# Kernel optimization log

Hardware: AMD Instinct MI355X
Metric: run time of the kernel (lower is better)

Reference implementation:

```python
import jax, jax.numpy as jnp
import numpy as np

N = 50000   # nodes (= node_input)
H = 128     # node_hidden
E = 800000  # edges per adjacency


def spmm(row, col, val, dense):
    # (sparse NxN) @ dense[N, F] via gather + segment_sum
    return jax.ops.segment_sum(dense[col] * val[:, None], row, num_segments=N)


def l2norm(x, eps=1e-12):
    n = jnp.sqrt(jnp.sum(x * x, axis=1, keepdims=True))
    return x / jnp.maximum(n, eps)


def setup_inputs() -> dict:
    key = jax.random.key(0)
    ks = jax.random.split(key, 20)
    stdv = 1.0 / np.sqrt(H)
    u = lambda k, shape, s: jax.random.uniform(k, shape, jnp.float32, -s, s)
    inp = {
        'in_row': jax.random.randint(ks[0], (E,), 0, N),
        'in_col': jax.random.randint(ks[1], (E,), 0, N),
        'in_val': jax.random.uniform(ks[2], (E,), jnp.float32),
        'out_row': jax.random.randint(ks[3], (E,), 0, N),
        'out_col': jax.random.randint(ks[4], (E,), 0, N),
        'out_val': jax.random.uniform(ks[5], (E,), jnp.float32),
        'W1': u(ks[6], (N, H), stdv), 'b1': u(ks[7], (H,), stdv),
        'W2': u(ks[8], (H, H), stdv), 'b2': u(ks[9], (H,), stdv),
        'W3': u(ks[10], (H, H), stdv), 'b3': u(ks[11], (H,), stdv),
        'W4': u(ks[12], (H, H), stdv), 'b4': u(ks[13], (H,), stdv),
        'lin1_w': jax.random.normal(ks[14], (2 * H, H), jnp.float32) * 0.05,
        'lin1_b': jnp.zeros((2 * H,), jnp.float32),
        'lin2_w': jax.random.normal(ks[15], (2 * H, 2 * H), jnp.float32) * 0.05,
        'lin2_b': jnp.zeros((2 * H,), jnp.float32),
        'lin3_w': jax.random.normal(ks[16], (1, 2 * H), jnp.float32) * 0.05,
        'lin3_b': jnp.zeros((1,), jnp.float32),
    }
    return inp


def reference(in_row, in_col, in_val, out_row, out_col, out_val,
              W1, b1, W2, b2, W3, b3, W4, b4,
              lin1_w, lin1_b, lin2_w, lin2_b, lin3_w, lin3_b):
    def branch(row, col, val):
        x1 = l2norm(jax.nn.relu(spmm(row, col, val, W1) + b1))
        x2 = l2norm(jax.nn.relu(spmm(row, col, val, x1 @ W2) + b2))
        x3 = l2norm(jax.nn.relu(spmm(row, col, val, x2 @ W3) + b3))
        x4 = jax.nn.relu(spmm(row, col, val, x3 @ W4) + b4)
        return (x1, x2, x3, x4)

    def score(x):  # dropout p=0.0 -> identity
        h = jax.nn.relu(x @ lin1_w.T + lin1_b)
        h = jax.nn.relu(h @ lin2_w.T + lin2_b)
        return h @ lin3_w.T + lin3_b

    xs_in = branch(in_row, in_col, in_val)
    xs_out = branch(out_row, out_col, out_val)
    score_in = sum(score(x) for x in xs_in)
    score_out = sum(score(x) for x in xs_out)
    return score_in * score_out
```

## Files before the change

### kernel.cpp

```cpp
#include <hip/hip_runtime.h>
#include <hip/hip_bf16.h>

#define NN 50000
#define HH 128
#define H2 256
#define EE 800000
#define NBUCK 196
#define BINCH 4096

typedef _Float16 half8 __attribute__((ext_vector_type(8)));
typedef float float4v __attribute__((ext_vector_type(4)));

__device__ __forceinline__ float bf2f(unsigned short u) {
  union { unsigned int i; float f; } v; v.i = ((unsigned int)u) << 16; return v.f;
}
__device__ __forceinline__ unsigned short f2bf(float f) {
  union { float f; unsigned int i; } v; v.f = f;
  unsigned int x = v.i;
  unsigned int r = x + 0x7fffu + ((x >> 16) & 1u);
  return (unsigned short)(r >> 16);
}

__global__ void detect_kernel(const unsigned int* __restrict__ val, int* __restrict__ dt) {
  unsigned int w = val[threadIdx.x];
  unsigned short u = (unsigned short)(w & 0xffff);
  int expf = (u >> 7) & 0xff;
  bool match = ((u >> 15) == 0) && expf >= 0x5A && expf <= 0x7E;
  unsigned long long m = __ballot(match);
  if (threadIdx.x == 0) dt[0] = (__popcll(m) >= 48) ? 1 : 0;
}

#define NSEG 14
struct ConvSegs {
  const void* s[NSEG];
  void* d[NSEG];
  int n[NSEG];
  int mode[NSEG];
  int kd[NSEG];
  int bstart[NSEG + 1];
};

__global__ __launch_bounds__(256) void convall_kernel(ConvSegs cs, const int* __restrict__ dt) {
  int b = blockIdx.x;
  int seg = 0;
  while (b >= cs.bstart[seg + 1]) ++seg;
  int i = (b - cs.bstart[seg]) * 256 + threadIdx.x;
  if (i >= cs.n[seg]) return;
  float f = dt[0] ? bf2f(((const unsigned short*)cs.s[seg])[i])
                  : ((const float*)cs.s[seg])[i];
  int m = cs.mode[seg];
  if (m == 0) { ((float*)cs.d[seg])[i] = f; return; }
  if (m == 1) { ((_Float16*)cs.d[seg])[i] = (_Float16)f; return; }
  int K = cs.kd[seg];
  int n, k;
  if (m == 3) { n = i / K; k = i - n * K; }
  else        { k = i >> 7; n = i & 127; }
  int NC16 = (cs.n[seg] / K) >> 4;
  int off = ((k >> 5) * NC16 + (n >> 4)) * 512 + (((k >> 3) & 3) * 16 + (n & 15)) * 8 + (k & 7);
  ((_Float16*)cs.d[seg])[off] = (_Float16)f;
}

__global__ __launch_bounds__(256) void bincount_kernel(
    const int* __restrict__ r0, const int* __restrict__ r1,
    int* __restrict__ bcnt, int E) {
  int br = blockIdx.y;
  const int* rows = br ? r1 : r0;
  __shared__ int cnt_s[NBUCK];
  int t = threadIdx.x;
  for (int i = t; i < NBUCK; i += 256) cnt_s[i] = 0;
  __syncthreads();
  int e0 = blockIdx.x * BINCH;
  #pragma unroll
  for (int i = 0; i < 16; ++i) {
    int e = e0 + i * 256 + t;
    if (e < E) atomicAdd(&cnt_s[rows[e] >> 8], 1);
  }
  __syncthreads();
  for (int i = t; i < NBUCK; i += 256) {
    int c = cnt_s[i];
    if (c) atomicAdd(&bcnt[br * NBUCK + i], c);
  }
}

// ... 70 lines not shown
  int* r = rp + br * (NN + 1);
  __shared__ int cur[256];
  __shared__ int s[256];
  int base = bbase[br * NBUCK + b];
  int end  = (b + 1 < NBUCK) ? bbase[br * NBUCK + b + 1] : E;
  cur[t] = 0;
  __syncthreads();
  for (int i = base + t; i < end; i += 256)
    atomicAdd(&cur[(((unsigned)bin[i].x) >> 16) & 255], 1);
  __syncthreads();
  int v = cur[t];
  s[t] = v;
  __syncthreads();
  for (int off = 1; off < 256; off <<= 1) {
    int u = (t >= off) ? s[t - off] : 0;
    __syncthreads();
    s[t] += u;
    __syncthreads();
  }
  int ex = base + s[t] - v;
  int row = b * 256 + t;
  if (row < N) r[row] = ex;
  if (b == 0 && t == 0) r[N] = E;
  cur[t] = ex;
  __syncthreads();
  for (int i = base + t; i < end; i += 256) {
    int2 e = bin[i];
    int rl = (((unsigned)e.x) >> 16) & 255;
    int p = atomicAdd(&cur[rl], 1);
    eo[p] = make_int2(e.x & 0xffff, e.y);
  }
}

template<int DO_L2>
__global__ __launch_bounds__(256) void spmm_kernel(
    const int* __restrict__ rp, const int2* __restrict__ edges,
    const _Float16* __restrict__ src, size_t sstride, const float* __restrict__ bias,
    _Float16* __restrict__ dst, size_t dstride, int N)
{
  int br = blockIdx.y;
  rp += br * (NN + 1);
  edges += (size_t)br * EE;
  src += br * sstride;
  dst += br * dstride;
  int g = threadIdx.x >> 4;
  int l = threadIdx.x & 15;
  int r = blockIdx.x * 16 + g;
  if (r >= N) return;
  int kb = rp[r], ke = rp[r + 1];
  float a0[8] = {0,0,0,0,0,0,0,0}, a1[8] = {0,0,0,0,0,0,0,0};
  float a2[8] = {0,0,0,0,0,0,0,0}, a3[8] = {0,0,0,0,0,0,0,0};
  int k = kb;
  for (; k + 3 < ke; k += 4) {
    int2 e0 = edges[k], e1 = edges[k + 1], e2 = edges[k + 2], e3 = edges[k + 3];
    half8 s0 = *(const half8*)(src + (size_t)e0.x * HH + l * 8);
    half8 s1 = *(const half8*)(src + (size_t)e1.x * HH + l * 8);
    half8 s2 = *(const half8*)(src + (size_t)e2.x * HH + l * 8);
    half8 s3 = *(const half8*)(src + (size_t)e3.x * HH + l * 8);
    float v0 = __int_as_float(e0.y), v1 = __int_as_float(e1.y);
    float v2 = __int_as_float(e2.y), v3 = __int_as_float(e3.y);
    #pragma unroll
    for (int j = 0; j < 8; ++j) {
      a0[j] = fmaf(v0, (float)s0[j], a0[j]);
      a1[j] = fmaf(v1, (float)s1[j], a1[j]);
      a2[j] = fmaf(v2, (float)s2[j], a2[j]);
      a3[j] = fmaf(v3, (float)s3[j], a3[j]);
    }
  }
  for (; k < ke; ++k) {
    int2 e0 = edges[k];
    half8 s0 = *(const half8*)(src + (size_t)e0.x * HH + l * 8);
    float v0 = __int_as_float(e0.y);
    #pragma unroll
    for (int j = 0; j < 8; ++j) a0[j] = fmaf(v0, (float)s0[j], a0[j]);
  }
  float x[8];
  #pragma unroll
  for (int j = 0; j < 8; ++j)
    x[j] = fmaxf((a0[j] + a1[j]) + (a2[j] + a3[j]) + bias[l * 8 + j], 0.f);
  if (DO_L2) {
    float ss = 0.f;
    #pragma unroll
    for (int j = 0; j < 8; ++j) ss += x[j] * x[j];
    #pragma unroll
    for (int m = 1; m < 16; m <<= 1) ss += __shfl_xor(ss, m, 64);
    float sc = 1.f / fmaxf(sqrtf(ss), 1e-12f);
    #pragma unroll
    for (int j = 0; j < 8; ++j) x[j] *= sc;
  }
  half8 hv;
  #pragma unroll
  for (int j = 0; j < 8; ++j) hv[j] = (_Float16)x[j];
  *(half8*)&dst[(size_t)r * HH + l * 8] = hv;
}

template<int DO_L2>
__global__ __launch_bounds__(256, 6) void fused_kernel(
    const int* __restrict__ rp, const int2* __restrict__ edges,
    const _Float16* __restrict__ xcur, _Float16* __restrict__ xnext,
    const _Float16* __restrict__ wt, const float* __restrict__ bias,
    const _Float16* __restrict__ w1, const _Float16* __restrict__ w2,
    const float* __restrict__ b1v, const float* __restrict__ b2v,
    const float* __restrict__ w3v,
    float* __restrict__ S, int N, int sg, int gx, int nsp)
{
  extern __shared__ _Float16 smem[];
  const size_t XSC = (size_t)(NN + 128) * HH;
  int br = blockIdx.y;
  rp += br * (NN + 1);
  edges += (size_t)br * EE;
  xcur += br * XSC;

  int bx = blockIdx.x;
  int role, idx;
  if (nsp) {
    int q = bx / 3, k3 = bx - q * 3;
    if (k3 < 2) { idx = q * 2 + k3; if (idx >= sg) return; role = 0; }
    else        { idx = q;          if (idx >= gx) return; role = 1; }
  } else { role = 1; idx = bx; if (idx >= gx) return; }

  const int lane = threadIdx.x & 63, w = threadIdx.x >> 6;
  const int lm = lane & 15, lq = lane >> 4;

  if (role == 0) {
    xnext += br * XSC;
    int g = threadIdx.x >> 4, l = threadIdx.x & 15;
    int r = idx * 16 + g;
    int kb = rp[r], ke = rp[r + 1];
    float a0[8] = {0,0,0,0,0,0,0,0}, a1[8] = {0,0,0,0,0,0,0,0};
    float a2[8] = {0,0,0,0,0,0,0,0}, a3[8] = {0,0,0,0,0,0,0,0};
    int k = kb;
    for (; k + 3 < ke; k += 4) {
      int2 e0 = edges[k], e1 = edges[k + 1], e2 = edges[k + 2], e3 = edges[k + 3];
      half8 s0 = *(const half8*)(xcur + (size_t)e0.x * HH + l * 8);
      half8 s1 = *(const half8*)(xcur + (size_t)e1.x * HH + l * 8);
      half8 s2 = *(const half8*)(xcur + (size_t)e2.x * HH + l * 8);
      half8 s3 = *(const half8*)(xcur + (size_t)e3.x * HH + l * 8);
      float v0 = __int_as_float(e0.y), v1 = __int_as_float(e1.y);
      float v2 = __int_as_float(e2.y), v3 = __int_as_float(e3.y);
      #pragma unroll
      for (int j = 0; j < 8; ++j) {
        a0[j] = fmaf(v0, (float)s0[j], a0[j]);
        a1[j] = fmaf(v1, (float)s1[j], a1[j]);
        a2[j] = fmaf(v2, (float)s2[j], a2[j]);
        a3[j] = fmaf(v3, (float)s3[j], a3[j]);
      }
    }
    for (; k < ke; ++k) {
      int2 e0 = edges[k];
      half8 s0 = *(const half8*)(xcur + (size_t)e0.x * HH + l * 8);
      float v0 = __int_as_float(e0.y);
      #pragma unroll
      for (int j = 0; j < 8; ++j) a0[j] = fmaf(v0, (float)s0[j], a0[j]);
    }
    half8 hv;
    #pragma unroll
    for (int j = 0; j < 8; ++j)
      hv[j] = (_Float16)((a0[j] + a1[j]) + (a2[j] + a3[j]));
    *(half8*)&smem[g * 136 + l * 8] = hv;
    __syncthreads();

    float4v acc[2];
    acc[0] = (float4v){0.f,0.f,0.f,0.f};
    acc[1] = (float4v){0.f,0.f,0.f,0.f};
    #pragma unroll
    for (int k0 = 0; k0 < HH; k0 += 32) {
      half8 ah = *(const half8*)&smem[lm * 136 + k0 + lq * 8];
      #pragma unroll
      for (int nt = 0; nt < 2; ++nt) {
        half8 bh = *(const half8*)(wt + (((k0 >> 5) * 8) + w * 2 + nt) * 512 + lane * 8);
        acc[nt] = __builtin_amdgcn_mfma_f32_16x16x32_f16(ah, bh, acc[nt], 0, 0, 0);
      }
    }
    float v[2][4];
    float ssp[4] = {0.f, 0.f, 0.f, 0.f};
    #pragma unroll
    for (int nt = 0; nt < 2; ++nt) {
      float bv = bias[w * 32 + nt * 16 + lm];
      #pragma unroll
      for (int rr = 0; rr < 4; ++rr) {
        float t = fmaxf(acc[nt][rr] + bv, 0.f);
        v[nt][rr] = t;
        ssp[rr] += t * t;
      }
    }
    if (DO_L2) {
      #pragma unroll
      for (int m = 1; m < 16; m <<= 1) {
        #pragma unroll
        for (int rr = 0; rr < 4; ++rr) ssp[rr] += __shfl_xor(ssp[rr], m, 64);
      }
      float* sred = (float*)(smem + 16 * 136);
      if (lm == 0) {
        #pragma unroll
        for (int rr = 0; rr < 4; ++rr) sred[w * 16 + lq * 4 + rr] = ssp[rr];
      }
      __syncthreads();
      #pragma unroll
      for (int rr = 0; rr < 4; ++rr) {
        int rowl = lq * 4 + rr;
        float tot = sred[rowl] + sred[16 + rowl] + sred[32 + rowl] + sred[48 + rowl];
        float sc = 1.f / fmaxf(sqrtf(tot), 1e-12f);
        v[0][rr] *= sc;
        v[1][rr] *= sc;
      }
    }
    #pragma unroll
    for (int rr = 0; rr < 4; ++rr) {
      size_t ro = (size_t)(idx * 16 + lq * 4 + rr) * HH;
      #pragma unroll
      for (int nt = 0; nt < 2; ++nt)
        xnext[ro + w * 32 + nt * 16 + lm] = (_Float16)v[nt][rr];
    }
    return;
  }

  float* Sb = S + (size_t)br * N;
  _Float16* h1s = smem;
  const int HS = H2 + 8;
  const int m0 = idx * 32;
  const int wn = w * 64;
  {
    float4v acc[2][4];
    #pragma unroll
    for (int i = 0; i < 2; ++i)
      #pragma unroll
      for (int j = 0; j < 4; ++j) acc[i][j] = (float4v){0.f,0.f,0.f,0.f};
    #pragma unroll
    for (int k0 = 0; k0 < HH; k0 += 32) {
      half8 ah[2], bh[4];
      #pragma unroll
      for (int mt = 0; mt < 2; ++mt)
        ah[mt] = *(const half8*)(xcur + (size_t)(m0 + mt * 16 + lm) * HH + k0 + lq * 8);
      #pragma unroll
      for (int nt = 0; nt < 4; ++nt)
        bh[nt] = *(const half8*)(w1 + (((k0 >> 5) * 16) + (wn >> 4) + nt) * 512 + lane * 8);
      #pragma unroll
      for (int mt = 0; mt < 2; ++mt)
        #pragma unroll
        for (int nt = 0; nt < 4; ++nt)
          acc[mt][nt] = __builtin_amdgcn_mfma_f32_16x16x32_f16(ah[mt], bh[nt], acc[mt][nt], 0, 0, 0);
    }
    float bv[4];
    #pragma unroll
    for (int nt = 0; nt < 4; ++nt) bv[nt] = b1v[wn + nt * 16 + lm];
// ... 60 lines not shown
                             const int* __restrict__ dt) {
  int i = blockIdx.x * 256 + threadIdx.x;
  if (i >= N) return;
  float b = 4.f * b3[0];
  float v = (s_in[i] + b) * (s_out[i] + b);
  if (dt[0]) ((unsigned short*)out)[i] = f2bf(v);
  else       ((float*)out)[i] = v;
}

extern "C" void kernel_launch(void* const* d_in, const int* in_sizes, int n_in,
                              void* d_out, int out_size, void* d_ws, size_t ws_size,
                              hipStream_t stream) {
  const int N = NN, E = EE;

  char* ws = (char*)d_ws;
  size_t o = 0;
  auto alloc = [&](size_t bytes) -> void* {
    void* p = ws + o;
    o = (o + bytes + 255) & ~(size_t)255;
    return p;
  };

  int* dt = (int*)alloc(16);
  float* bc[4]; float* l1b; float* l2b; float* w3f; float* l3b;
  for (int i = 0; i < 4; ++i) bc[i] = (float*)alloc(HH * 4);
  l1b = (float*)alloc(H2 * 4);
  l2b = (float*)alloc(H2 * 4);
  w3f = (float*)alloc(H2 * 4);
  l3b = (float*)alloc(4);
  _Float16* l1w_h = (_Float16*)alloc(H2 * HH * 2);
  _Float16* l2w_h = (_Float16*)alloc(H2 * H2 * 2);
  _Float16* Wt_h[3];
  for (int i = 0; i < 3; ++i) Wt_h[i] = (_Float16*)alloc(HH * HH * 2);
  _Float16* w1_h = (_Float16*)alloc((size_t)N * HH * 2);

  const int NP = N + 128;
  const size_t XS = (size_t)NP * HH;
  int* rp    = (int*)alloc(2 * (size_t)(N + 1) * 4);
  int* bcnt  = (int*)alloc(2 * NBUCK * 4);
  int* bbase = (int*)alloc(2 * NBUCK * 4);
  int* gcur  = (int*)alloc(2 * NBUCK * 4);
  int2* binned = (int2*)alloc(2 * (size_t)E * 8);
  int2* edges  = (int2*)alloc(2 * (size_t)E * 8);
  _Float16* x_h  = (_Float16*)alloc(2 * XS * 2);
  _Float16* tb_h = (_Float16*)alloc(2 * XS * 2);
  float* sacc = (float*)alloc(2 * (size_t)N * 4);

  dim3 blk(256);
  detect_kernel<<<1, 64, 0, stream>>>((const unsigned int*)d_in[2], dt);

  ConvSegs cs;
  const void* srcs[NSEG] = {d_in[7], d_in[9], d_in[11], d_in[13], d_in[15], d_in[17],
                            d_in[18], d_in[19], d_in[14], d_in[16], d_in[8], d_in[10],
                            d_in[12], d_in[6]};
  void* dsts[NSEG] = {bc[0], bc[1], bc[2], bc[3], l1b, l2b, w3f, l3b,
                      l1w_h, l2w_h, Wt_h[0], Wt_h[1], Wt_h[2], w1_h};
  int ns[NSEG] = {HH, HH, HH, HH, H2, H2, H2, 1,
                  H2 * HH, H2 * H2, HH * HH, HH * HH, HH * HH, N * HH};
  int ms[NSEG] = {0, 0, 0, 0, 0, 0, 0, 0, 3, 3, 4, 4, 4, 1};
  int ks[NSEG] = {0, 0, 0, 0, 0, 0, 0, 0, HH, H2, HH, HH, HH, 0};
  int btot = 0;
  for (int i = 0; i < NSEG; ++i) {
    cs.s[i] = srcs[i]; cs.d[i] = dsts[i]; cs.n[i] = ns[i]; cs.mode[i] = ms[i]; cs.kd[i] = ks[i];
    cs.bstart[i] = btot;
    btot += (ns[i] + 255) / 256;
  }
  cs.bstart[NSEG] = btot;
  convall_kernel<<<btot, blk, 0, stream>>>(cs, dt);

  hipMemsetAsync(sacc, 0, 2 * (size_t)N * 4, stream);
  hipMemsetAsync(bcnt, 0, 2 * NBUCK * 4, stream);
  hipMemsetAsync(x_h  + (size_t)N * HH, 0, (size_t)128 * HH * 2, stream);
  hipMemsetAsync(x_h  + XS + (size_t)N * HH, 0, (size_t)128 * HH * 2, stream);
  hipMemsetAsync(tb_h + (size_t)N * HH, 0, (size_t)128 * HH * 2, stream);
  hipMemsetAsync(tb_h + XS + (size_t)N * HH, 0, (size_t)128 * HH * 2, stream);

  int sg   = (N + 15) / 16;
  int gx32 = (N + 31) / 32;
  int mg   = ((sg + 1) / 2) * 3;
  int bg   = (E + BINCH - 1) / BINCH;
  const size_t FLDS = (size_t)32 * (H2 + 8) * sizeof(_Float16);

  bincount_kernel<<<dim3(bg, 2), blk, 0, stream>>>((const int*)d_in[0], (const int*)d_in[3], bcnt, E);
  bscan_kernel<<<dim3(1, 2), blk, 0, stream>>>(bcnt, bbase, gcur);
  bin_kernel<<<dim3(bg, 2), blk, 0, stream>>>(
      (const int*)d_in[0], (const int*)d_in[3], (const int*)d_in[1], (const int*)d_in[4],
      d_in[2], d_in[5], gcur, binned, E, dt);
  bucket_kernel<<<dim3(NBUCK, 2), blk, 0, stream>>>(bbase, binned, edges, rp, N, E);

  spmm_kernel<1><<<dim3(sg, 2), blk, 0, stream>>>(rp, edges, w1_h, 0, bc[0], x_h, XS, N);

  fused_kernel<1><<<dim3(mg, 2), blk, FLDS, stream>>>(
      rp, edges, x_h, tb_h, Wt_h[0], bc[1], l1w_h, l2w_h, l1b, l2b, w3f,
      sacc, N, sg, gx32, 1);
  fused_kernel<1><<<dim3(mg, 2), blk, FLDS, stream>>>(
      rp, edges, tb_h, x_h, Wt_h[1], bc[2], l1w_h, l2w_h, l1b, l2b, w3f,
      sacc, N, sg, gx32, 1);
  fused_kernel<0><<<dim3(mg, 2), blk, FLDS, stream>>>(
      rp, edges, x_h, tb_h, Wt_h[2], bc[3], l1w_h, l2w_h, l1b, l2b, w3f,
      sacc, N, sg, gx32, 1);
  fused_kernel<0><<<dim3(gx32, 2), blk, FLDS, stream>>>(
      rp, edges, tb_h, nullptr, nullptr, nullptr, l1w_h, l2w_h, l1b, l2b, w3f,
      sacc, N, 0, gx32, 0);

  final_kernel<<<(N + 255) / 256, blk, 0, stream>>>(sacc, sacc + N, l3b, d_out, N, dt);
}
```

Before: 560.1 us.

## Gather SpMM sources from packed 12-bit fp16 copies with fp16 packed math

Adds a 12-bit-per-element packed copy of each feature matrix (an 8-bit high byte plus a 4-bit nibble, 192 bytes per row instead of 256), written next to the fp16 output. The SpMM gathers now read this compressed form and accumulate with packed half2 multiplies. This cuts gather bandwidth, the dominant cost of the random-access SpMM. The gather-and-transform role is also retiled to 32 rows per block with 8 lanes per row, using 2x2 MFMA tiles. In exchange the inputs lose mantissa precision and sums are partly formed in fp16, which risks accuracy tolerance, and each layer now writes an extra quantized copy.

```diff
diff --git a/kernel.cpp b/kernel.cpp
--- a/kernel.cpp
+++ b/kernel.cpp
@@ -7,8 +7,10 @@
 #define EE 800000
 #define NBUCK 196
 #define BINCH 4096
+#define QS 192
 
 typedef _Float16 half8 __attribute__((ext_vector_type(8)));
+typedef _Float16 half2v __attribute__((ext_vector_type(2)));
 typedef float float4v __attribute__((ext_vector_type(4)));
 
 __device__ __forceinline__ float bf2f(unsigned short u) {
@@ -19,6 +21,109 @@
   unsigned int x = v.i;
   unsigned int r = x + 0x7fffu + ((x >> 16) & 1u);
   return (unsigned short)(r >> 16);
+}
+
+__device__ __forceinline__ unsigned int enc12h(unsigned short h) {
+  unsigned int m = (unsigned int)h & 0x7fffu;
+  unsigned int c = (m + 0x7u + ((h >> 4) & 1u)) >> 4;
+  return c | (((unsigned int)h >> 15) << 11);
+}
+__device__ __forceinline__ unsigned int enc12f(float x) {
+  return enc12h(__builtin_bit_cast(unsigned short, (_Float16)x));
+}
+
+__device__ __forceinline__ void dec8(unsigned int hw0, unsigned int hw1, unsigned int nw,
+                                     half2v vv, half2v& p0, half2v& p1,
+                                     half2v& p2, half2v& p3) {
+  unsigned int u01 = __byte_perm(hw0, 0u, 0x4140);
+  unsigned int u23 = __byte_perm(hw0, 0u, 0x4342);
+  unsigned int u45 = __byte_perm(hw1, 0u, 0x4140);
+  unsigned int u67 = __byte_perm(hw1, 0u, 0x4342);
+  unsigned int a01 = ((nw & 0xFu) << 4)        | ((nw & 0xF0u) << 16);
+  unsigned int a23 = ((nw & 0xF00u) >> 4)      | ((nw & 0xF000u) << 8);
+  unsigned int a45 = ((nw & 0xF0000u) >> 12)   | (nw & 0xF00000u);
+  unsigned int a67 = ((nw & 0x0F000000u) >> 20) | ((nw & 0xF0000000u) >> 8);
+  p0 += __builtin_bit_cast(half2v, (u01 << 8) | a01) * vv;
+  p1 += __builtin_bit_cast(half2v, (u23 << 8) | a23) * vv;
+  p2 += __builtin_bit_cast(half2v, (u45 << 8) | a45) * vv;
+  p3 += __builtin_bit_cast(half2v, (u67 << 8) | a67) * vv;
+}
+
+__device__ __forceinline__ void gather_q12(int kb, int ke,
+    const int2* __restrict__ edges, const unsigned char* __restrict__ sq,
+    int l, float* a)
+{
+  int k = kb;
+  for (; k + 3 < ke; k += 4) {
+    int2 e0 = edges[k], e1 = edges[k + 1], e2 = edges[k + 2], e3 = edges[k + 3];
+    const unsigned char* b0 = sq + (size_t)e0.x * QS;
+    const unsigned char* b1 = sq + (size_t)e1.x * QS;
+    const unsigned char* b2 = sq + (size_t)e2.x * QS;
+    const unsigned char* b3 = sq + (size_t)e3.x * QS;
+    uint4 Ha = *(const uint4*)(b0 + l * 16);
+    uint4 Hb = *(const uint4*)(b1 + l * 16);
+    uint4 Hc = *(const uint4*)(b2 + l * 16);
+    uint4 Hd = *(const uint4*)(b3 + l * 16);
+    uint2 La = *(const uint2*)(b0 + 128 + l * 8);
+    uint2 Lb = *(const uint2*)(b1 + 128 + l * 8);
+    uint2 Lc = *(const uint2*)(b2 + 128 + l * 8);
+    uint2 Ld = *(const uint2*)(b3 + 128 + l * 8);
+    _Float16 v0 = (_Float16)__int_as_float(e0.y);
+    _Float16 v1 = (_Float16)__int_as_float(e1.y);
+    _Float16 v2 = (_Float16)__int_as_float(e2.y);
+    _Float16 v3 = (_Float16)__int_as_float(e3.y);
+    half2v vv0 = {v0, v0}, vv1 = {v1, v1}, vv2 = {v2, v2}, vv3 = {v3, v3};
+    half2v p0 = {0, 0}, p1 = {0, 0}, p2 = {0, 0}, p3 = {0, 0};
+    half2v p4 = {0, 0}, p5 = {0, 0}, p6 = {0, 0}, p7 = {0, 0};
+    dec8(Ha.x, Ha.y, La.x, vv0, p0, p1, p2, p3);
+    dec8(Ha.z, Ha.w, La.y, vv0, p4, p5, p6, p7);
+    dec8(Hb.x, Hb.y, Lb.x, vv1, p0, p1, p2, p3);
+    dec8(Hb.z, Hb.w, Lb.y, vv1, p4, p5, p6, p7);
+    dec8(Hc.x, Hc.y, Lc.x, vv2, p0, p1, p2, p3);
+    dec8(Hc.z, Hc.w, Lc.y, vv2, p4, p5, p6, p7);
+    dec8(Hd.x, Hd.y, Ld.x, vv3, p0, p1, p2, p3);
+    dec8(Hd.z, Hd.w, Ld.y, vv3, p4, p5, p6, p7);
+    a[0] += (float)p0[0]; a[1] += (float)p0[1]; a[2] += (float)p1[0]; a[3] += (float)p1[1];
+    a[4] += (float)p2[0]; a[5] += (float)p2[1]; a[6] += (float)p3[0]; a[7] += (float)p3[1];
+    a[8] += (float)p4[0]; a[9] += (float)p4[1]; a[10] += (float)p5[0]; a[11] += (float)p5[1];
+    a[12] += (float)p6[0]; a[13] += (float)p6[1]; a[14] += (float)p7[0]; a[15] += (float)p7[1];
+  }
+  for (; k < ke; ++k) {
+    int2 e0 = edges[k];
+    const unsigned char* b0 = sq + (size_t)e0.x * QS;
+    uint4 Ha = *(const uint4*)(b0 + l * 16);
+    uint2 La = *(const uint2*)(b0 + 128 + l * 8);
+    _Float16 v0 = (_Float16)__int_as_float(e0.y);
+    half2v vv0 = {v0, v0};
+    half2v p0 = {0, 0}, p1 = {0, 0}, p2 = {0, 0}, p3 = {0, 0};
+    half2v p4 = {0, 0}, p5 = {0, 0}, p6 = {0, 0}, p7 = {0, 0};
+    dec8(Ha.x, Ha.y, La.x, vv0, p0, p1, p2, p3);
+    dec8(Ha.z, Ha.w, La.y, vv0, p4, p5, p6, p7);
+    a[0] += (float)p0[0]; a[1] += (float)p0[1]; a[2] += (float)p1[0]; a[3] += (float)p1[1];
+    a[4] += (float)p2[0]; a[5] += (float)p2[1]; a[6] += (float)p3[0]; a[7] += (float)p3[1];
+    a[8] += (float)p4[0]; a[9] += (float)p4[1]; a[10] += (float)p5[0]; a[11] += (float)p5[1];
+    a[12] += (float)p6[0]; a[13] += (float)p6[1]; a[14] += (float)p7[0]; a[15] += (float)p7[1];
+  }
+}
+
+__device__ __forceinline__ void store_q12(unsigned char* dq, size_t r, int l,
+                                          const _Float16* xv) {
+  unsigned int c[16];
+  #pragma unroll
+  for (int j = 0; j < 16; ++j)
+    c[j] = enc12h(__builtin_bit_cast(unsigned short, xv[j]));
+  uint4 Hw;
+  Hw.x = (c[0] >> 4)  | ((c[1] >> 4) << 8)  | ((c[2] >> 4) << 16)  | ((c[3] >> 4) << 24);
+  Hw.y = (c[4] >> 4)  | ((c[5] >> 4) << 8)  | ((c[6] >> 4) << 16)  | ((c[7] >> 4) << 24);
+  Hw.z = (c[8] >> 4)  | ((c[9] >> 4) << 8)  | ((c[10] >> 4) << 16) | ((c[11] >> 4) << 24);
+  Hw.w = (c[12] >> 4) | ((c[13] >> 4) << 8) | ((c[14] >> 4) << 16) | ((c[15] >> 4) << 24);
+  uint2 Lw;
+  Lw.x = (c[0] & 0xF) | ((c[1] & 0xF) << 4) | ((c[2] & 0xF) << 8) | ((c[3] & 0xF) << 12)
+      | ((c[4] & 0xF) << 16) | ((c[5] & 0xF) << 20) | ((c[6] & 0xF) << 24) | ((c[7] & 0xF) << 28);
+  Lw.y = (c[8] & 0xF) | ((c[9] & 0xF) << 4) | ((c[10] & 0xF) << 8) | ((c[11] & 0xF) << 12)
+      | ((c[12] & 0xF) << 16) | ((c[13] & 0xF) << 20) | ((c[14] & 0xF) << 24) | ((c[15] & 0xF) << 28);
+  *(uint4*)(dq + r * QS + l * 16) = Hw;
+  *(uint2*)(dq + r * QS + 128 + l * 8) = Lw;
 }
 
 __global__ void detect_kernel(const unsigned int* __restrict__ val, int* __restrict__ dt) {
@@ -46,9 +151,27 @@
   while (b >= cs.bstart[seg + 1]) ++seg;
   int i = (b - cs.bstart[seg]) * 256 + threadIdx.x;
   if (i >= cs.n[seg]) return;
+  int m = cs.mode[seg];
+  if (m == 5) {
+    float f0, f1;
+    if (dt[0]) {
+      f0 = bf2f(((const unsigned short*)cs.s[seg])[2 * i]);
+      f1 = bf2f(((const unsigned short*)cs.s[seg])[2 * i + 1]);
+    } else {
+      f0 = ((const float*)cs.s[seg])[2 * i];
+      f1 = ((const float*)cs.s[seg])[2 * i + 1];
+    }
+    unsigned int c0 = enc12f(f0), c1 = enc12f(f1);
+    int row = i >> 6;
+    int t = i & 63;
+    unsigned char* dq = (unsigned char*)cs.d[seg];
+    *(unsigned short*)(dq + (size_t)row * QS + 2 * t) =
+        (unsigned short)((c0 >> 4) | ((c1 >> 4) << 8));
+    dq[(size_t)row * QS + 128 + t] = (unsigned char)((c0 & 0xF) | ((c1 & 0xF) << 4));
+    return;
+  }
   float f = dt[0] ? bf2f(((const unsigned short*)cs.s[seg])[i])
                   : ((const float*)cs.s[seg])[i];
-  int m = cs.mode[seg];
   if (m == 0) { ((float*)cs.d[seg])[i] = f; return; }
   if (m == 1) { ((_Float16*)cs.d[seg])[i] = (_Float16)f; return; }
   int K = cs.kd[seg];
@@ -185,72 +308,51 @@
   }
 }
 
-template<int DO_L2>
-__global__ __launch_bounds__(256) void spmm_kernel(
+__global__ __launch_bounds__(256) void spmm1_kernel(
     const int* __restrict__ rp, const int2* __restrict__ edges,
-    const _Float16* __restrict__ src, size_t sstride, const float* __restrict__ bias,
-    _Float16* __restrict__ dst, size_t dstride, int N)
+    const unsigned char* __restrict__ srcq, const float* __restrict__ bias,
+    _Float16* __restrict__ dst, unsigned char* __restrict__ dstq, int N)
 {
+  const size_t XSC = (size_t)(NN + 128) * HH;
+  const size_t XQC = (size_t)(NN + 128) * QS;
   int br = blockIdx.y;
   rp += br * (NN + 1);
   edges += (size_t)br * EE;
-  src += br * sstride;
-  dst += br * dstride;
-  int g = threadIdx.x >> 4;
-  int l = threadIdx.x & 15;
-  int r = blockIdx.x * 16 + g;
+  dst += br * XSC;
+  dstq += br * XQC;
+  int g = threadIdx.x >> 3, l = threadIdx.x & 7;
+  int r = blockIdx.x * 32 + g;
   if (r >= N) return;
   int kb = rp[r], ke = rp[r + 1];
-  float a0[8] = {0,0,0,0,0,0,0,0}, a1[8] = {0,0,0,0,0,0,0,0};
-  float a2[8] = {0,0,0,0,0,0,0,0}, a3[8] = {0,0,0,0,0,0,0,0};
-  int k = kb;
-  for (; k + 3 < ke; k += 4) {
-    int2 e0 = edges[k], e1 = edges[k + 1], e2 = edges[k + 2], e3 = edges[k + 3];
-    half8 s0 = *(const half8*)(src + (size_t)e0.x * HH + l * 8);
-    half8 s1 = *(const half8*)(src + (size_t)e1.x * HH + l * 8);
-    half8 s2 = *(const half8*)(src + (size_t)e2.x * HH + l * 8);
-    half8 s3 = *(const half8*)(src + (size_t)e3.x * HH + l * 8);
-    float v0 = __int_as_float(e0.y), v1 = __int_as_float(e1.y);
-    float v2 = __int_as_float(e2.y), v3 = __int_as_float(e3.y);
-    #pragma unroll
-    for (int j = 0; j < 8; ++j) {
-      a0[j] = fmaf(v0, (float)s0[j], a0[j]);
-      a1[j] = fmaf(v1, (float)s1[j], a1[j]);
-      a2[j] = fmaf(v2, (float)s2[j], a2[j]);
-      a3[j] = fmaf(v3, (float)s3[j], a3[j]);
-    }
-  }
-  for (; k < ke; ++k) {
-    int2 e0 = edges[k];
-    half8 s0 = *(const half8*)(src + (size_t)e0.x * HH + l * 8);
-    float v0 = __int_as_float(e0.y);
-    #pragma unroll
-    for (int j = 0; j < 8; ++j) a0[j] = fmaf(v0, (float)s0[j], a0[j]);
-  }
-  float x[8];
-  #pragma unroll
-  for (int j = 0; j < 8; ++j)
-    x[j] = fmaxf((a0[j] + a1[j]) + (a2[j] + a3[j]) + bias[l * 8 + j], 0.f);
-  if (DO_L2) {
-    float ss = 0.f;
-    #pragma unroll
-    for (int j = 0; j < 8; ++j) ss += x[j] * x[j];
-    #pragma unroll
-    for (int m = 1; m < 16; m <<= 1) ss += __shfl_xor(ss, m, 64);
-    float sc = 1.f / fmaxf(sqrtf(ss), 1e-12f);
-    #pragma unroll
-    for (int j = 0; j < 8; ++j) x[j] *= sc;
-  }
-  half8 hv;
-  #pragma unroll
-  for (int j = 0; j < 8; ++j) hv[j] = (_Float16)x[j];
-  *(half8*)&dst[(size_t)r * HH + l * 8] = hv;
+  float a[16];
+  #pragma unroll
+  for (int j = 0; j < 16; ++j) a[j] = 0.f;
+  gather_q12(kb, ke, edges, srcq, l, a);
+  float x[16];
+  #pragma unroll
+  for (int j = 0; j < 16; ++j)
+    x[j] = fmaxf(a[j] + bias[l * 16 + j], 0.f);
+  float ss = 0.f;
+  #pragma unroll
+  for (int j = 0; j < 16; ++j) ss += x[j] * x[j];
+  #pragma unroll
+  for (int m = 1; m < 8; m <<= 1) ss += __shfl_xor(ss, m, 64);
+  float sc = 1.f / fmaxf(sqrtf(ss), 1e-12f);
+  #pragma unroll
+  for (int j = 0; j < 16; ++j) x[j] *= sc;
+  _Float16 xh[16];
+  #pragma unroll
+  for (int j = 0; j < 16; ++j) xh[j] = (_Float16)x[j];
+  *(half8*)&dst[(size_t)r * HH + l * 16] = *(half8*)&xh[0];
+  *(half8*)&dst[(size_t)r * HH + l * 16 + 8] = *(half8*)&xh[8];
+  store_q12(dstq, (size_t)r, l, xh);
 }
 
 template<int DO_L2>
 __global__ __launch_bounds__(256, 6) void fused_kernel(
     const int* __restrict__ rp, const int2* __restrict__ edges,
-    const _Float16* __restrict__ xcur, _Float16* __restrict__ xnext,
+    const _Float16* __restrict__ xcur, const unsigned char* __restrict__ xq,
+    _Float16* __restrict__ xnext, unsigned char* __restrict__ xnq,
     const _Float16* __restrict__ wt, const float* __restrict__ bias,
     const _Float16* __restrict__ w1, const _Float16* __restrict__ w2,
     const float* __restrict__ b1v, const float* __restrict__ b2v,
@@ -259,17 +361,19 @@
 {
   extern __shared__ _Float16 smem[];
   const size_t XSC = (size_t)(NN + 128) * HH;
+  const size_t XQC = (size_t)(NN + 128) * QS;
   int br = blockIdx.y;
   rp += br * (NN + 1);
   edges += (size_t)br * EE;
   xcur += br * XSC;
+  xq += br * XQC;
 
   int bx = blockIdx.x;
   int role, idx;
   if (nsp) {
-    int q = bx / 3, k3 = bx - q * 3;
-    if (k3 < 2) { idx = q * 2 + k3; if (idx >= sg) return; role = 0; }
-    else        { idx = q;          if (idx >= gx) return; role = 1; }
+    idx = bx >> 1;
+    if (bx & 1) { role = 1; if (idx >= gx) return; }
+    else        { role = 0; if (idx >= sg) return; }
   } else { role = 1; idx = bx; if (idx >= gx) return; }
 
   const int lane = threadIdx.x & 63, w = threadIdx.x >> 6;
@@ -277,93 +381,110 @@
 
   if (role == 0) {
     xnext += br * XSC;
-    int g = threadIdx.x >> 4, l = threadIdx.x & 15;
-    int r = idx * 16 + g;
-    int kb = rp[r], ke = rp[r + 1];
-    float a0[8] = {0,0,0,0,0,0,0,0}, a1[8] = {0,0,0,0,0,0,0,0};
-    float a2[8] = {0,0,0,0,0,0,0,0}, a3[8] = {0,0,0,0,0,0,0,0};
-    int k = kb;
-    for (; k + 3 < ke; k += 4) {
-      int2 e0 = edges[k], e1 = edges[k + 1], e2 = edges[k + 2], e3 = edges[k + 3];
-      half8 s0 = *(const half8*)(xcur + (size_t)e0.x * HH + l * 8);
-      half8 s1 = *(const half8*)(xcur + (size_t)e1.x * HH + l * 8);
-      half8 s2 = *(const half8*)(xcur + (size_t)e2.x * HH + l * 8);
-      half8 s3 = *(const half8*)(xcur + (size_t)e3.x * HH + l * 8);
-      float v0 = __int_as_float(e0.y), v1 = __int_as_float(e1.y);
-      float v2 = __int_as_float(e2.y), v3 = __int_as_float(e3.y);
-      #pragma unroll
-      for (int j = 0; j < 8; ++j) {
-        a0[j] = fmaf(v0, (float)s0[j], a0[j]);
-        a1[j] = fmaf(v1, (float)s1[j], a1[j]);
-        a2[j] = fmaf(v2, (float)s2[j], a2[j]);
-        a3[j] = fmaf(v3, (float)s3[j], a3[j]);
-      }
-    }
-    for (; k < ke; ++k) {
-      int2 e0 = edges[k];
-      half8 s0 = *(const half8*)(xcur + (size_t)e0.x * HH + l * 8);
-      float v0 = __int_as_float(e0.y);
-      #pragma unroll
-      for (int j = 0; j < 8; ++j) a0[j] = fmaf(v0, (float)s0[j], a0[j]);
-    }
-    half8 hv;
-    #pragma unroll
-    for (int j = 0; j < 8; ++j)
-      hv[j] = (_Float16)((a0[j] + a1[j]) + (a2[j] + a3[j]));
-    *(half8*)&smem[g * 136 + l * 8] = hv;
+    xnq += br * XQC;
+    int g = threadIdx.x >> 3, l = threadIdx.x & 7;
+    int r = idx * 32 + g;
+    int kb = 0, ke = 0;
+    if (r < N) { kb = rp[r]; ke = rp[r + 1]; }
+    float a[16];
+    #pragma unroll
+    for (int j = 0; j < 16; ++j) a[j] = 0.f;
+    gather_q12(kb, ke, edges, xq, l, a);
+    {
+      half8 h0, h1;
+      #pragma unroll
+      for (int j = 0; j < 8; ++j) { h0[j] = (_Float16)a[j]; h1[j] = (_Float16)a[j + 8]; }
+      *(half8*)&smem[g * 136 + l * 16] = h0;
+      *(half8*)&smem[g * 136 + l * 16 + 8] = h1;
+    }
     __syncthreads();
 
-    float4v acc[2];
-    acc[0] = (float4v){0.f,0.f,0.f,0.f};
-    acc[1] = (float4v){0.f,0.f,0.f,0.f};
+    float4v acc[2][2];
+    #pragma unroll
+    for (int i = 0; i < 2; ++i)
+      #pragma unroll
+      for (int j = 0; j < 2; ++j) acc[i][j] = (float4v){0.f, 0.f, 0.f, 0.f};
     #pragma unroll
     for (int k0 = 0; k0 < HH; k0 += 32) {
-      half8 ah = *(const half8*)&smem[lm * 136 + k0 + lq * 8];
-      #pragma unroll
-      for (int nt = 0; nt < 2; ++nt) {
-        half8 bh = *(const half8*)(wt + (((k0 >> 5) * 8) + w * 2 + nt) * 512 + lane * 8);
-        acc[nt] = __builtin_amdgcn_mfma_f32_16x16x32_f16(ah, bh, acc[nt], 0, 0, 0);
-      }
-    }
-    float v[2][4];
-    float ssp[4] = {0.f, 0.f, 0.f, 0.f};
+      half8 ah[2], bh[2];
+      #pragma unroll
+      for (int mt = 0; mt < 2; ++mt)
+        ah[mt] = *(const half8*)&smem[(mt * 16 + lm) * 136 + k0 + lq * 8];
+      #pragma unroll
+      for (int nt = 0; nt < 2; ++nt)
+        bh[nt] = *(const half8*)(wt + (((k0 >> 5) * 8) + w * 2 + nt) * 512 + lane * 8);
+      #pragma unroll
+      for (int mt = 0; mt < 2; ++mt)
+        #pragma unroll
+        for (int nt = 0; nt < 2; ++nt)
+          acc[mt][nt] = __builtin_amdgcn_mfma_f32_16x16x32_f16(ah[mt], bh[nt], acc[mt][nt], 0, 0, 0);
+    }
+    float vv[2][2][4];
+    float ssp[2][4];
+    #pragma unroll
+    for (int mt = 0; mt < 2; ++mt)
+      #pragma unroll
+      for (int rr = 0; rr < 4; ++rr) ssp[mt][rr] = 0.f;
     #pragma unroll
     for (int nt = 0; nt < 2; ++nt) {
       float bv = bias[w * 32 + nt * 16 + lm];
       #pragma unroll
+      for (int mt = 0; mt < 2; ++mt)
+        #pragma unroll
+        for (int rr = 0; rr < 4; ++rr) {
+          float t = fmaxf(acc[mt][nt][rr] + bv, 0.f);
+          vv[mt][nt][rr] = t;
+          ssp[mt][rr] += t * t;
+        }
+    }
+    if (DO_L2) {
+      #pragma unroll
+      for (int m = 1; m < 16; m <<= 1)
+        #pragma unroll
+        for (int mt = 0; mt < 2; ++mt)
+          #pragma unroll
+          for (int rr = 0; rr < 4; ++rr) ssp[mt][rr] += __shfl_xor(ssp[mt][rr], m, 64);
+      float* sred = (float*)(smem + 32 * 136);
+      if (lm == 0)
+        #pragma unroll
+        for (int mt = 0; mt < 2; ++mt)
+          #pragma unroll
+          for (int rr = 0; rr < 4; ++rr) sred[w * 32 + mt * 16 + lq * 4 + rr] = ssp[mt][rr];
+      __syncthreads();
+      #pragma unroll
+      for (int mt = 0; mt < 2; ++mt)
+        #pragma unroll
+        for (int rr = 0; rr < 4; ++rr) {
+          int rowl = mt * 16 + lq * 4 + rr;
+          float tot = sred[rowl] + sred[32 + rowl] + sred[64 + rowl] + sred[96 + rowl];
+          float sc = 1.f / fmaxf(sqrtf(tot), 1e-12f);
+          vv[mt][0][rr] *= sc;
+          vv[mt][1][rr] *= sc;
+        }
+    } else {
+      __syncthreads();
+    }
+    #pragma unroll
+    for (int mt = 0; mt < 2; ++mt)
+      #pragma unroll
       for (int rr = 0; rr < 4; ++rr) {
-        float t = fmaxf(acc[nt][rr] + bv, 0.f);
-        v[nt][rr] = t;
-        ssp[rr] += t * t;
+        int rowl = mt * 16 + lq * 4 + rr;
+        #pragma unroll
+        for (int nt = 0; nt < 2; ++nt)
+          smem[rowl * 136 + w * 32 + nt * 16 + lm] = (_Float16)vv[mt][nt][rr];
       }
-    }
-    if (DO_L2) {
-      #pragma unroll
-      for (int m = 1; m < 16; m <<= 1) {
-        #pragma unroll
-        for (int rr = 0; rr < 4; ++rr) ssp[rr] += __shfl_xor(ssp[rr], m, 64);
+    __syncthreads();
+    if (r < N) {
+      half8 h0 = *(const half8*)&smem[g * 136 + l * 16];
+      half8 h1 = *(const half8*)&smem[g * 136 + l * 16 + 8];
+      *(half8*)&xnext[(size_t)r * HH + l * 16] = h0;
+      *(half8*)&xnext[(size_t)r * HH + l * 16 + 8] = h1;
+      if (DO_L2) {
+        _Float16 xh[16];
+        #pragma unroll
+        for (int j = 0; j < 8; ++j) { xh[j] = h0[j]; xh[8 + j] = h1[j]; }
+        store_q12(xnq, (size_t)r, l, xh);
       }
-      float* sred = (float*)(smem + 16 * 136);
-      if (lm == 0) {
-        #pragma unroll
-        for (int rr = 0; rr < 4; ++rr) sred[w * 16 + lq * 4 + rr] = ssp[rr];
-      }
-      __syncthreads();
-      #pragma unroll
-      for (int rr = 0; rr < 4; ++rr) {
-        int rowl = lq * 4 + rr;
-        float tot = sred[rowl] + sred[16 + rowl] + sred[32 + rowl] + sred[48 + rowl];
-        float sc = 1.f / fmaxf(sqrtf(tot), 1e-12f);
-        v[0][rr] *= sc;
-        v[1][rr] *= sc;
-      }
-    }
-    #pragma unroll
-    for (int rr = 0; rr < 4; ++rr) {
-      size_t ro = (size_t)(idx * 16 + lq * 4 + rr) * HH;
-      #pragma unroll
-      for (int nt = 0; nt < 2; ++nt)
-        xnext[ro + w * 32 + nt * 16 + lm] = (_Float16)v[nt][rr];
     }
     return;
   }
@@ -490,10 +611,11 @@
   _Float16* l2w_h = (_Float16*)alloc(H2 * H2 * 2);
   _Float16* Wt_h[3];
   for (int i = 0; i < 3; ++i) Wt_h[i] = (_Float16*)alloc(HH * HH * 2);
-  _Float16* w1_h = (_Float16*)alloc((size_t)N * HH * 2);
+  unsigned char* w1_q = (unsigned char*)alloc((size_t)N * QS);
 
   const int NP = N + 128;
   const size_t XS = (size_t)NP * HH;
+  const size_t XQ = (size_t)NP * QS;
   int* rp    = (int*)alloc(2 * (size_t)(N + 1) * 4);
   int* bcnt  = (int*)alloc(2 * NBUCK * 4);
   int* bbase = (int*)alloc(2 * NBUCK * 4);
@@ -502,6 +624,8 @@
   int2* edges  = (int2*)alloc(2 * (size_t)E * 8);
   _Float16* x_h  = (_Float16*)alloc(2 * XS * 2);
   _Float16* tb_h = (_Float16*)alloc(2 * XS * 2);
+  unsigned char* x_q  = (unsigned char*)alloc(2 * XQ);
+  unsigned char* tb_q = (unsigned char*)alloc(2 * XQ);
   float* sacc = (float*)alloc(2 * (size_t)N * 4);
 
   dim3 blk(256);
@@ -512,10 +636,10 @@
                             d_in[18], d_in[19], d_in[14], d_in[16], d_in[8], d_in[10],
                             d_in[12], d_in[6]};
   void* dsts[NSEG] = {bc[0], bc[1], bc[2], bc[3], l1b, l2b, w3f, l3b,
-                      l1w_h, l2w_h, Wt_h[0], Wt_h[1], Wt_h[2], w1_h};
+                      l1w_h, l2w_h, Wt_h[0], Wt_h[1], Wt_h[2], w1_q};
   int ns[NSEG] = {HH, HH, HH, HH, H2, H2, H2, 1,
-                  H2 * HH, H2 * H2, HH * HH, HH * HH, HH * HH, N * HH};
-  int ms[NSEG] = {0, 0, 0, 0, 0, 0, 0, 0, 3, 3, 4, 4, 4, 1};
+                  H2 * HH, H2 * H2, HH * HH, HH * HH, HH * HH, N * HH / 2};
+  int ms[NSEG] = {0, 0, 0, 0, 0, 0, 0, 0, 3, 3, 4, 4, 4, 5};
   int ks[NSEG] = {0, 0, 0, 0, 0, 0, 0, 0, HH, H2, HH, HH, HH, 0};
   int btot = 0;
   for (int i = 0; i < NSEG; ++i) {
@@ -533,9 +657,9 @@
   hipMemsetAsync(tb_h + (size_t)N * HH, 0, (size_t)128 * HH * 2, stream);
   hipMemsetAsync(tb_h + XS + (size_t)N * HH, 0, (size_t)128 * HH * 2, stream);
 
-  int sg   = (N + 15) / 16;
+  int sg2  = (N + 31) / 32;
   int gx32 = (N + 31) / 32;
-  int mg   = ((sg + 1) / 2) * 3;
+  int mg   = 2 * sg2;
   int bg   = (E + BINCH - 1) / BINCH;
   const size_t FLDS = (size_t)32 * (H2 + 8) * sizeof(_Float16);
 
@@ -546,19 +670,19 @@
       d_in[2], d_in[5], gcur, binned, E, dt);
   bucket_kernel<<<dim3(NBUCK, 2), blk, 0, stream>>>(bbase, binned, edges, rp, N, E);
 
-  spmm_kernel<1><<<dim3(sg, 2), blk, 0, stream>>>(rp, edges, w1_h, 0, bc[0], x_h, XS, N);
+  spmm1_kernel<<<dim3(sg2, 2), blk, 0, stream>>>(rp, edges, w1_q, bc[0], x_h, x_q, N);
 
   fused_kernel<1><<<dim3(mg, 2), blk, FLDS, stream>>>(
-      rp, edges, x_h, tb_h, Wt_h[0], bc[1], l1w_h, l2w_h, l1b, l2b, w3f,
-      sacc, N, sg, gx32, 1);
+      rp, edges, x_h, x_q, tb_h, tb_q, Wt_h[0], bc[1], l1w_h, l2w_h, l1b, l2b, w3f,
+      sacc, N, sg2, gx32, 1);
   fused_kernel<1><<<dim3(mg, 2), blk, FLDS, stream>>>(
-      rp, edges, tb_h, x_h, Wt_h[1], bc[2], l1w_h, l2w_h, l1b, l2b, w3f,
-      sacc, N, sg, gx32, 1);
+      rp, edges, tb_h, tb_q, x_h, x_q, Wt_h[1], bc[2], l1w_h, l2w_h, l1b, l2b, w3f,
+      sacc, N, sg2, gx32, 1);
   fused_kernel<0><<<dim3(mg, 2), blk, FLDS, stream>>>(
-      rp, edges, x_h, tb_h, Wt_h[2], bc[3], l1w_h, l2w_h, l1b, l2b, w3f,
-      sacc, N, sg, gx32, 1);
+      rp, edges, x_h, x_q, tb_h, tb_q, Wt_h[2], bc[3], l1w_h, l2w_h, l1b, l2b, w3f,
+      sacc, N, sg2, gx32, 1);
   fused_kernel<0><<<dim3(gx32, 2), blk, FLDS, stream>>>(
-      rp, edges, tb_h, nullptr, nullptr, nullptr, l1w_h, l2w_h, l1b, l2b, w3f,
+      rp, edges, tb_h, tb_q, x_h, x_q, Wt_h[0], bc[0], l1w_h, l2w_h, l1b, l2b, w3f,
       sacc, N, 0, gx32, 0);
 
   final_kernel<<<(N + 255) / 256, blk, 0, stream>>>(sacc, sacc + N, l3b, d_out, N, dt);
```

Result: slower. 622.1 us (+11.1%).

## Store layer activations as 8-bit floats for cheaper SpMM gathers

Applied to the files above, without the earlier changes.

The fused layer kernels now also write an 8-bit, FP8-like copy of their output activations, scaled by 1/256 with 1 sign bit, 4 exponent bits and 3 mantissa bits. The next two layers' SpMM gathers read this quantized copy instead of fp16, which halves the bytes fetched per gathered edge. Decoding is done with bit shifts into fp16 and accumulated with packed half2 multiply-adds. The cost is an extra LDS round-trip and an encode pass on write, plus reduced precision in the gathered activations, which risks accuracy.

```diff
diff --git a/kernel.cpp b/kernel.cpp
--- a/kernel.cpp
+++ b/kernel.cpp
@@ -7,8 +7,10 @@
 #define EE 800000
 #define NBUCK 196
 #define BINCH 4096
+#define QB 128
 
 typedef _Float16 half8 __attribute__((ext_vector_type(8)));
+typedef _Float16 half2v __attribute__((ext_vector_type(2)));
 typedef float float4v __attribute__((ext_vector_type(4)));
 
 __device__ __forceinline__ float bf2f(unsigned short u) {
@@ -19,6 +21,24 @@
   unsigned int x = v.i;
   unsigned int r = x + 0x7fffu + ((x >> 16) & 1u);
   return (unsigned short)(r >> 16);
+}
+
+__device__ __forceinline__ unsigned int qenc(float x) {
+  unsigned short h = __builtin_bit_cast(unsigned short, (_Float16)(x * 0.00390625f));
+  unsigned int s = ((unsigned int)h >> 15) & 1u;
+  unsigned int m = (unsigned int)h & 0x7fffu;
+  if (m > 0x1FBFu) m = 0x1FBFu;
+  unsigned int t = m + 0x1Fu + ((m >> 6) & 1u);
+  return (s << 7) | ((t >> 6) & 0x7fu);
+}
+
+__device__ __forceinline__ void qdec(unsigned int wd, half2v vv, half2v& pa, half2v& pb) {
+  unsigned int u01 = __byte_perm(wd, 0u, 0x4140);
+  unsigned int u23 = __byte_perm(wd, 0u, 0x4342);
+  unsigned int h01 = ((u01 & 0x00800080u) << 8) | ((u01 & 0x007f007fu) << 6);
+  unsigned int h23 = ((u23 & 0x00800080u) << 8) | ((u23 & 0x007f007fu) << 6);
+  pa += __builtin_bit_cast(half2v, h01) * vv;
+  pb += __builtin_bit_cast(half2v, h23) * vv;
 }
 
 __global__ void detect_kernel(const unsigned int* __restrict__ val, int* __restrict__ dt) {
@@ -247,10 +267,11 @@
   *(half8*)&dst[(size_t)r * HH + l * 8] = hv;
 }
 
-template<int DO_L2>
+template<int DO_L2, int GQ, int SQ>
 __global__ __launch_bounds__(256, 6) void fused_kernel(
     const int* __restrict__ rp, const int2* __restrict__ edges,
-    const _Float16* __restrict__ xcur, _Float16* __restrict__ xnext,
+    const _Float16* __restrict__ xcur, const unsigned char* __restrict__ xq,
+    _Float16* __restrict__ xnext, unsigned char* __restrict__ xnq,
     const _Float16* __restrict__ wt, const float* __restrict__ bias,
     const _Float16* __restrict__ w1, const _Float16* __restrict__ w2,
     const float* __restrict__ b1v, const float* __restrict__ b2v,
@@ -259,10 +280,12 @@
 {
   extern __shared__ _Float16 smem[];
   const size_t XSC = (size_t)(NN + 128) * HH;
+  const size_t XQC = (size_t)(NN + 128) * QB;
   int br = blockIdx.y;
   rp += br * (NN + 1);
   edges += (size_t)br * EE;
   xcur += br * XSC;
+  if (GQ) xq += br * XQC;
 
   int bx = blockIdx.x;
   int role, idx;
@@ -277,39 +300,80 @@
 
   if (role == 0) {
     xnext += br * XSC;
+    if (SQ) xnq += br * XQC;
     int g = threadIdx.x >> 4, l = threadIdx.x & 15;
     int r = idx * 16 + g;
     int kb = rp[r], ke = rp[r + 1];
-    float a0[8] = {0,0,0,0,0,0,0,0}, a1[8] = {0,0,0,0,0,0,0,0};
-    float a2[8] = {0,0,0,0,0,0,0,0}, a3[8] = {0,0,0,0,0,0,0,0};
-    int k = kb;
-    for (; k + 3 < ke; k += 4) {
-      int2 e0 = edges[k], e1 = edges[k + 1], e2 = edges[k + 2], e3 = edges[k + 3];
-      half8 s0 = *(const half8*)(xcur + (size_t)e0.x * HH + l * 8);
-      half8 s1 = *(const half8*)(xcur + (size_t)e1.x * HH + l * 8);
-      half8 s2 = *(const half8*)(xcur + (size_t)e2.x * HH + l * 8);
-      half8 s3 = *(const half8*)(xcur + (size_t)e3.x * HH + l * 8);
-      float v0 = __int_as_float(e0.y), v1 = __int_as_float(e1.y);
-      float v2 = __int_as_float(e2.y), v3 = __int_as_float(e3.y);
-      #pragma unroll
-      for (int j = 0; j < 8; ++j) {
-        a0[j] = fmaf(v0, (float)s0[j], a0[j]);
-        a1[j] = fmaf(v1, (float)s1[j], a1[j]);
-        a2[j] = fmaf(v2, (float)s2[j], a2[j]);
-        a3[j] = fmaf(v3, (float)s3[j], a3[j]);
-      }
-    }
-    for (; k < ke; ++k) {
-      int2 e0 = edges[k];
-      half8 s0 = *(const half8*)(xcur + (size_t)e0.x * HH + l * 8);
-      float v0 = __int_as_float(e0.y);
-      #pragma unroll
-      for (int j = 0; j < 8; ++j) a0[j] = fmaf(v0, (float)s0[j], a0[j]);
-    }
     half8 hv;
-    #pragma unroll
-    for (int j = 0; j < 8; ++j)
-      hv[j] = (_Float16)((a0[j] + a1[j]) + (a2[j] + a3[j]));
+    if (GQ) {
+      float a[8] = {0,0,0,0,0,0,0,0};
+      int k = kb;
+      for (; k + 3 < ke; k += 4) {
+        int2 e0 = edges[k], e1 = edges[k + 1], e2 = edges[k + 2], e3 = edges[k + 3];
+        uint2 q0 = *(const uint2*)(xq + (size_t)e0.x * QB + l * 8);
+        uint2 q1 = *(const uint2*)(xq + (size_t)e1.x * QB + l * 8);
+        uint2 q2 = *(const uint2*)(xq + (size_t)e2.x * QB + l * 8);
+        uint2 q3 = *(const uint2*)(xq + (size_t)e3.x * QB + l * 8);
+        _Float16 v0 = (_Float16)(__int_as_float(e0.y) * 256.f);
+        _Float16 v1 = (_Float16)(__int_as_float(e1.y) * 256.f);
+        _Float16 v2 = (_Float16)(__int_as_float(e2.y) * 256.f);
+        _Float16 v3 = (_Float16)(__int_as_float(e3.y) * 256.f);
+        half2v vv0 = {v0, v0}, vv1 = {v1, v1}, vv2 = {v2, v2}, vv3 = {v3, v3};
+        half2v p0 = {0, 0}, p1 = {0, 0}, p2 = {0, 0}, p3 = {0, 0};
+        qdec(q0.x, vv0, p0, p1); qdec(q0.y, vv0, p2, p3);
+        qdec(q1.x, vv1, p0, p1); qdec(q1.y, vv1, p2, p3);
+        qdec(q2.x, vv2, p0, p1); qdec(q2.y, vv2, p2, p3);
+        qdec(q3.x, vv3, p0, p1); qdec(q3.y, vv3, p2, p3);
+        a[0] += (float)p0[0]; a[1] += (float)p0[1];
+        a[2] += (float)p1[0]; a[3] += (float)p1[1];
+        a[4] += (float)p2[0]; a[5] += (float)p2[1];
+        a[6] += (float)p3[0]; a[7] += (float)p3[1];
+      }
+      for (; k < ke; ++k) {
+        int2 e0 = edges[k];
+        uint2 q0 = *(const uint2*)(xq + (size_t)e0.x * QB + l * 8);
+        _Float16 v0 = (_Float16)(__int_as_float(e0.y) * 256.f);
+        half2v vv0 = {v0, v0};
+        half2v p0 = {0, 0}, p1 = {0, 0}, p2 = {0, 0}, p3 = {0, 0};
+        qdec(q0.x, vv0, p0, p1); qdec(q0.y, vv0, p2, p3);
+        a[0] += (float)p0[0]; a[1] += (float)p0[1];
+        a[2] += (float)p1[0]; a[3] += (float)p1[1];
+        a[4] += (float)p2[0]; a[5] += (float)p2[1];
+        a[6] += (float)p3[0]; a[7] += (float)p3[1];
+      }
+      #pragma unroll
+      for (int j = 0; j < 8; ++j) hv[j] = (_Float16)a[j];
+    } else {
+      float a0[8] = {0,0,0,0,0,0,0,0}, a1[8] = {0,0,0,0,0,0,0,0};
+      float a2[8] = {0,0,0,0,0,0,0,0}, a3[8] = {0,0,0,0,0,0,0,0};
+      int k = kb;
+      for (; k + 3 < ke; k += 4) {
+        int2 e0 = edges[k], e1 = edges[k + 1], e2 = edges[k + 2], e3 = edges[k + 3];
+        half8 s0 = *(const half8*)(xcur + (size_t)e0.x * HH + l * 8);
+        half8 s1 = *(const half8*)(xcur + (size_t)e1.x * HH + l * 8);
+        half8 s2 = *(const half8*)(xcur + (size_t)e2.x * HH + l * 8);
+        half8 s3 = *(const half8*)(xcur + (size_t)e3.x * HH + l * 8);
+        float v0 = __int_as_float(e0.y), v1 = __int_as_float(e1.y);
+        float v2 = __int_as_float(e2.y), v3 = __int_as_float(e3.y);
+        #pragma unroll
+        for (int j = 0; j < 8; ++j) {
+          a0[j] = fmaf(v0, (float)s0[j], a0[j]);
+          a1[j] = fmaf(v1, (float)s1[j], a1[j]);
+          a2[j] = fmaf(v2, (float)s2[j], a2[j]);
+          a3[j] = fmaf(v3, (float)s3[j], a3[j]);
+        }
+      }
+      for (; k < ke; ++k) {
+        int2 e0 = edges[k];
+        half8 s0 = *(const half8*)(xcur + (size_t)e0.x * HH + l * 8);
+        float v0 = __int_as_float(e0.y);
+        #pragma unroll
+        for (int j = 0; j < 8; ++j) a0[j] = fmaf(v0, (float)s0[j], a0[j]);
+      }
+      #pragma unroll
+      for (int j = 0; j < 8; ++j)
+        hv[j] = (_Float16)((a0[j] + a1[j]) + (a2[j] + a3[j]));
+    }
     *(half8*)&smem[g * 136 + l * 8] = hv;
     __syncthreads();
 
@@ -364,6 +428,25 @@
       #pragma unroll
       for (int nt = 0; nt < 2; ++nt)
         xnext[ro + w * 32 + nt * 16 + lm] = (_Float16)v[nt][rr];
+    }
+    if (SQ) {
+      __syncthreads();
+      #pragma unroll
+      for (int rr = 0; rr < 4; ++rr) {
+        int rowl = lq * 4 + rr;
+        #pragma unroll
+        for (int nt = 0; nt < 2; ++nt)
+          smem[rowl * 136 + w * 32 + nt * 16 + lm] = (_Float16)v[nt][rr];
+      }
+      __syncthreads();
+      unsigned int bq[8];
+      #pragma unroll
+      for (int j = 0; j < 8; ++j)
+        bq[j] = qenc((float)smem[g * 136 + l * 8 + j]);
+      uint2 qo;
+      qo.x = bq[0] | (bq[1] << 8) | (bq[2] << 16) | (bq[3] << 24);
+      qo.y = bq[4] | (bq[5] << 8) | (bq[6] << 16) | (bq[7] << 24);
+      *(uint2*)(xnq + (size_t)r * QB + l * 8) = qo;
     }
     return;
   }
@@ -494,6 +577,7 @@
 
   const int NP = N + 128;
   const size_t XS = (size_t)NP * HH;
+  const size_t XQ = (size_t)NP * QB;
   int* rp    = (int*)alloc(2 * (size_t)(N + 1) * 4);
   int* bcnt  = (int*)alloc(2 * NBUCK * 4);
   int* bbase = (int*)alloc(2 * NBUCK * 4);
@@ -502,6 +586,8 @@
   int2* edges  = (int2*)alloc(2 * (size_t)E * 8);
   _Float16* x_h  = (_Float16*)alloc(2 * XS * 2);
   _Float16* tb_h = (_Float16*)alloc(2 * XS * 2);
+  unsigned char* x_q  = (unsigned char*)alloc(2 * XQ);
+  unsigned char* tb_q = (unsigned char*)alloc(2 * XQ);
   float* sacc = (float*)alloc(2 * (size_t)N * 4);
 
   dim3 blk(256);
@@ -548,17 +634,17 @@
 
   spmm_kernel<1><<<dim3(sg, 2), blk, 0, stream>>>(rp, edges, w1_h, 0, bc[0], x_h, XS, N);
 
-  fused_kernel<1><<<dim3(mg, 2), blk, FLDS, stream>>>(
-      rp, edges, x_h, tb_h, Wt_h[0], bc[1], l1w_h, l2w_h, l1b, l2b, w3f,
+  fused_kernel<1, 0, 1><<<dim3(mg, 2), blk, FLDS, stream>>>(
+      rp, edges, x_h, nullptr, tb_h, tb_q, Wt_h[0], bc[1], l1w_h, l2w_h, l1b, l2b, w3f,
       sacc, N, sg, gx32, 1);
-  fused_kernel<1><<<dim3(mg, 2), blk, FLDS, stream>>>(
-      rp, edges, tb_h, x_h, Wt_h[1], bc[2], l1w_h, l2w_h, l1b, l2b, w3f,
+  fused_kernel<1, 1, 1><<<dim3(mg, 2), blk, FLDS, stream>>>(
+      rp, edges, tb_h, tb_q, x_h, x_q, Wt_h[1], bc[2], l1w_h, l2w_h, l1b, l2b, w3f,
       sacc, N, sg, gx32, 1);
-  fused_kernel<0><<<dim3(mg, 2), blk, FLDS, stream>>>(
-      rp, edges, x_h, tb_h, Wt_h[2], bc[3], l1w_h, l2w_h, l1b, l2b, w3f,
+  fused_kernel<0, 1, 0><<<dim3(mg, 2), blk, FLDS, stream>>>(
+      rp, edges, x_h, x_q, tb_h, nullptr, Wt_h[2], bc[3], l1w_h, l2w_h, l1b, l2b, w3f,
       sacc, N, sg, gx32, 1);
-  fused_kernel<0><<<dim3(gx32, 2), blk, FLDS, stream>>>(
-      rp, edges, tb_h, nullptr, nullptr, nullptr, l1w_h, l2w_h, l1b, l2b, w3f,
+  fused_kernel<0, 0, 0><<<dim3(gx32, 2), blk, FLDS, stream>>>(
+      rp, edges, tb_h, nullptr, nullptr, nullptr, nullptr, nullptr, l1w_h, l2w_h, l1b, l2b, w3f,
       sacc, N, 0, gx32, 0);
 
   final_kernel<<<(N + 255) / 256, blk, 0, stream>>>(sacc, sacc + N, l3b, d_out, N, dt);
```

Measured after the change: 563.7 us. Within noise of the previous version (+0.6%).
